# Kernel optimization log

Hardware: AMD Instinct MI355X
Metric: run time of the kernel (lower is better)

## Reference

```python
import jax, jax.numpy as jnp
import numpy as np
import math

B, S, D, H = 2, 2048, 2048, 16
HD = D // H  # head_dim = 128
NEG = -9e15


def setup_inputs() -> dict:
    key = jax.random.key(0)
    k1, k2, k3 = jax.random.split(key, 3)
    x = jax.random.normal(k1, (B, S, D), dtype=jnp.float32)
    Wqkv = jax.random.normal(k2, (D, 3 * D), dtype=jnp.float32) * (1.0 / math.sqrt(D))
    bqkv = jnp.zeros((3 * D,), dtype=jnp.float32)
    Wo = jax.random.normal(k3, (D, D), dtype=jnp.float32) * (1.0 / math.sqrt(D))
    bo = jnp.zeros((D,), dtype=jnp.float32)
    return {"x": x, "Wqkv": Wqkv, "bqkv": bqkv, "Wo": Wo, "bo": bo}


def reference(x, Wqkv, bqkv, Wo, bo):
    b, s, d = x.shape
    # fused QKV projection
    qkv = x @ Wqkv + bqkv                       # [B,S,3D]
    qkv = qkv.reshape(b, s, H, 3 * HD)          # per-head interleaved q|k|v
    qkv = qkv.transpose(0, 2, 1, 3)             # [B,H,S,3*HD]
    q, k, v = jnp.split(qkv, 3, axis=-1)        # each [B,H,S,HD]
    scale = 1.0 / math.sqrt(HD)
    logits = jnp.einsum('bhqd,bhkd->bhqk', q, k) * scale  # [B,H,S,S]
    causal = jnp.tril(jnp.ones((s, s), dtype=bool))[None, None]
    logits = jnp.where(causal, logits, NEG)
    score = jax.nn.softmax(logits, axis=-1)
    attn = jnp.einsum('bhqk,bhkd->bhqd', score, v)         # [B,H,S,HD]
    attn = attn.transpose(0, 2, 1, 3).reshape(b, s, d)
    return attn @ Wo + bo
```

## Files before the change

kernel.cpp:

```cpp
#include <hip/hip_runtime.h>
#include <stdint.h>

#define DEV static __device__ __forceinline__

typedef _Float16 half8 __attribute__((ext_vector_type(8)));
typedef _Float16 half4 __attribute__((ext_vector_type(4)));
typedef float f32x4 __attribute__((ext_vector_type(4)));

constexpr int Bc = 2, Sc = 2048, Dc = 2048, Hc = 16, HDc = 128;
constexpr int D3c = 3 * Dc;
constexpr int Mc = Bc * Sc;

DEV void gl_lds16(const void* g, void* l) {
    __builtin_amdgcn_global_load_lds(
        (const __attribute__((address_space(1))) unsigned int*)g,
        (__attribute__((address_space(3))) unsigned int*)l,
        16, 0, 0);
}

DEV void transpose_tile(const float* __restrict__ in, _Float16* __restrict__ out,
                        int R, int C, int bx, int by, float (*ls)[65], int t)
{
    const int r0 = by * 64, c0 = bx * 64;
    const int rr = t >> 6, cc = t & 63;
#pragma unroll
    for (int i = 0; i < 16; ++i) {
        int r = i * 4 + rr;
        ls[r][cc] = in[(size_t)(r0 + r) * C + c0 + cc];
    }
    __syncthreads();
#pragma unroll
    for (int i = 0; i < 16; ++i) {
        int r = i * 4 + rr;
        out[(size_t)(c0 + r) * R + r0 + cc] = (_Float16)ls[cc][r];
    }
}

__global__ __launch_bounds__(256) void preproc_kernel(
    const float* __restrict__ x, const float* __restrict__ Wqkv,
    const float* __restrict__ Wo,
    _Float16* __restrict__ xb, _Float16* __restrict__ wt1, _Float16* __restrict__ wt2)
{
    __shared__ float ls[64][65];
    const int bid = blockIdx.x, t = threadIdx.x;
    if (bid < 4096) {
        int i = bid * 256 + t;
        const float4* p = (const float4*)x;
        float4 a = p[i * 2], b = p[i * 2 + 1];
        half8 hv;
        hv[0] = (_Float16)a.x; hv[1] = (_Float16)a.y; hv[2] = (_Float16)a.z; hv[3] = (_Float16)a.w;
        hv[4] = (_Float16)b.x; hv[5] = (_Float16)b.y; hv[6] = (_Float16)b.z; hv[7] = (_Float16)b.w;
        *(half8*)(xb + (size_t)i * 8) = hv;
    } else if (bid < 4096 + 3072) {
        int tb = bid - 4096;
        transpose_tile(Wqkv, wt1, Dc, D3c, tb % 96, tb / 96, ls, t);
    } else {
        int tb = bid - 7168;
        transpose_tile(Wo, wt2, Dc, Dc, tb & 31, tb >> 5, ls, t);
    }
}

__global__ __launch_bounds__(256) void transpose_v_kernel(
    const uint16_t* __restrict__ qkv, uint16_t* __restrict__ vt)
{
    __shared__ uint32_t ls[64][65];
    const int t = threadIdx.x;
    const int s0 = blockIdx.x * 64, d0 = blockIdx.y * 64, bh = blockIdx.z;
    const int b = bh >> 4, h = bh & 15;
    const int rr = t >> 6, cc = t & 63;
#pragma unroll
    for (int i = 0; i < 16; ++i) {
        int r = i * 4 + rr;
        ls[r][cc] = qkv[(size_t)(b * Sc + s0 + r) * D3c + h * 384 + 256 + d0 + cc];
    }
    __syncthreads();
#pragma unroll
    for (int i = 0; i < 16; ++i) {
        int r = i * 4 + rr;
        vt[(size_t)(bh * HDc + d0 + r) * Sc + s0 + cc] = (uint16_t)ls[cc][r];
    }
}

template <int BF16OUT>
__global__ __launch_bounds__(256, 2) void gemm_bt_kernel(
    const _Float16* __restrict__ A, const _Float16* __restrict__ Bt,
    const float* __restrict__ bias, void* __restrict__ Cout,
    int M, int N, int K)
{
    __shared__ __align__(16) char smem[32768];
    char* sA = smem;
    char* sB = smem + 16384;
    const int t = threadIdx.x, w = t >> 6, lane = t & 63;
    const int quad = lane >> 4, l15 = lane & 15;
    const int wr = w >> 1, wc = w & 1;
    const int n0 = blockIdx.x * 128, m0 = blockIdx.y * 128;

    const f32x4 vzero = {0.f, 0.f, 0.f, 0.f};
    f32x4 acc[4][4];
#pragma unroll
    for (int i = 0; i < 4; ++i)
#pragma unroll
        for (int j = 0; j < 4; ++j) acc[i][j] = vzero;

    const int kiters = K >> 6;
    for (int kk = 0; kk < kiters; ++kk) {
#pragma unroll
        for (int i = 0; i < 4; ++i) {
            int c = i * 256 + t;
            int row = c >> 3, kbs = c & 7, kact = kbs ^ (row & 7);
            gl_lds16(A + (size_t)(m0 + row) * K + kk * 64 + kact * 8,
                     sA + (i * 256 + w * 64) * 16);
        }
#pragma unroll
        for (int i = 0; i < 4; ++i) {
            int c = i * 256 + t;
            int row = c >> 3, kbs = c & 7, kact = kbs ^ (row & 7);
            gl_lds16(Bt + (size_t)(n0 + row) * K + kk * 64 + kact * 8,
                     sB + (i * 256 + w * 64) * 16);
        }
        __syncthreads();
#pragma unroll
        for (int ks = 0; ks < 2; ++ks) {
            half8 af[4], bf[4];
#pragma unroll
            for (int mt = 0; mt < 4; ++mt) {
                int row = wr * 64 + mt * 16 + l15;
                int kact = (ks * 4 + quad) ^ (l15 & 7);
                af[mt] = *(const half8*)(sA + row * 128 + kact * 16);
            }
#pragma unroll
            for (int nt = 0; nt < 4; ++nt) {
                int row = wc * 64 + nt * 16 + l15;
                int kact = (ks * 4 + quad) ^ (l15 & 7);
                bf[nt] = *(const half8*)(sB + row * 128 + kact * 16);
            }
#pragma unroll
            for (int mt = 0; mt < 4; ++mt)
#pragma unroll
                for (int nt = 0; nt < 4; ++nt)
                    acc[mt][nt] = __builtin_amdgcn_mfma_f32_16x16x32_f16(
                        af[mt], bf[nt], acc[mt][nt], 0, 0, 0);
        }
        __syncthreads();
    }

#pragma unroll
    for (int nt = 0; nt < 4; ++nt) {
        int col = n0 + wc * 64 + nt * 16 + l15;
        float bv = bias[col];
#pragma unroll
        for (int mt = 0; mt < 4; ++mt)
#pragma unroll
            for (int r = 0; r < 4; ++r) {
                int row = m0 + wr * 64 + mt * 16 + quad * 4 + r;
                float v = acc[mt][nt][r] + bv;
                if (BF16OUT) ((_Float16*)Cout)[(size_t)row * N + col] = (_Float16)v;
                else         ((float*)Cout)[(size_t)row * N + col] = v;
            }
    }
}

__global__ __launch_bounds__(256, 3) void flash_kernel(
    const _Float16* __restrict__ qkv, const _Float16* __restrict__ vt,
    _Float16* __restrict__ attn)
{
    __shared__ __align__(16) char smem[34816];
    char* sK = smem;
    char* sV = smem + 16384;

    const int t = threadIdx.x, w = t >> 6, lane = t & 63;
    const int quad = lane >> 4, l15 = lane & 15;
    const int bh = blockIdx.x;
    const int qt = 15 - blockIdx.y;
    const int b = bh >> 4, h = bh & 15;
    const int q0 = qt * 128;
    const int qw = q0 + w * 32;

    half8 qf[2][4];
#pragma unroll
    for (int g = 0; g < 2; ++g)
#pragma unroll
        for (int ks = 0; ks < 4; ++ks) {
            const _Float16* p = qkv + (size_t)(b * Sc + qw + g * 16 + l15) * D3c +
                                h * 384 + ks * 32 + quad * 8;
            qf[g][ks] = *(const half8*)p;
        }

    const f32x4 vzero = {0.f, 0.f, 0.f, 0.f};
    f32x4 o[2][8];
#pragma unroll
    for (int g = 0; g < 2; ++g)
#pragma unroll
        for (int dt = 0; dt < 8; ++dt) o[g][dt] = vzero;
    float m_st[2] = {-1e30f, -1e30f}, l_st[2] = {0.f, 0.f};

    const float kScale = 0.08838834764831845f * 1.4426950408889634f;
    const int nkt = 2 * qt + 2;
    const int nkt_w = (qw + 95) >> 6;

    for (int kt = 0; kt < nkt; ++kt) {
#pragma unroll
        for (int i = 0; i < 4; ++i) {
            int c = i * 256 + t;
            int row = c >> 4, kbs = c & 15, kact = kbs ^ (row & 15);
            gl_lds16(qkv + (size_t)(b * Sc + kt * 64 + row) * D3c + h * 384 + 128 + kact * 8,
                     sK + (i * 256 + w * 64) * 16);
        }
#pragma unroll
        for (int i = 0; i < 4; ++i) {
            int c = i * 256 + t;
            int row = c >> 3, kbs = c & 7, kact = kbs ^ (row & 7);
            gl_lds16(vt + (size_t)(bh * HDc + row) * Sc + kt * 64 + kact * 8,
                     sV + (i * 256 + w * 64) * 16);
        }
        __syncthreads();

        if (kt < nkt_w) {
            f32x4 sf[2][4];
#pragma unroll
            for (int g = 0; g < 2; ++g)
#pragma unroll
                for (int kb = 0; kb < 4; ++kb) sf[g][kb] = vzero;
#pragma unroll
            for (int ks = 0; ks < 4; ++ks) {
#pragma unroll
                for (int kb = 0; kb < 4; ++kb) {
                    int row = kb * 16 + l15;
                    int slot = (ks * 4 + quad) ^ l15;
                    half8 kf = *(const half8*)(sK + row * 256 + slot * 16);
                    sf[0][kb] = __builtin_amdgcn_mfma_f32_16x16x32_f16(kf, qf[0][ks], sf[0][kb], 0, 0, 0);
                    sf[1][kb] = __builtin_amdgcn_mfma_f32_16x16x32_f16(kf, qf[1][ks], sf[1][kb], 0, 0, 0);
                }
            }

            half4 pb[2][4];
#pragma unroll
            for (int g = 0; g < 2; ++g) {
                const int qcol = qw + g * 16 + l15;
                const bool domask = (kt * 64 + 63 > qw + g * 16);
                float rm = -1e30f;
#pragma unroll
                for (int kb = 0; kb < 4; ++kb)
#pragma unroll
                    for (int r = 0; r < 4; ++r) {
                        float v = sf[g][kb][r] * kScale;
                        if (domask) {
                            int col = kt * 64 + kb * 16 + quad * 4 + r;
                            if (col > qcol) v = -1e30f;
                        }
                        sf[g][kb][r] = v;
                        rm = fmaxf(rm, v);
                    }
                rm = fmaxf(rm, __shfl_xor(rm, 16, 64));
                rm = fmaxf(rm, __shfl_xor(rm, 32, 64));
                float mn = fmaxf(m_st[g], rm);
                float alpha = __builtin_amdgcn_exp2f(m_st[g] - mn);
                m_st[g] = mn;

                float rs = 0.f;
#pragma unroll
                for (int kb = 0; kb < 4; ++kb)
#pragma unroll
                    for (int r = 0; r < 4; ++r) {
                        float p = __builtin_amdgcn_exp2f(sf[g][kb][r] - mn);
                        rs += p;
                        pb[g][kb][r] = (_Float16)p;
                    }
                rs += __shfl_xor(rs, 16, 64);
                rs += __shfl_xor(rs, 32, 64);
                l_st[g] = l_st[g] * alpha + rs;
#pragma unroll
                for (int dt = 0; dt < 8; ++dt)
#pragma unroll
                    for (int r = 0; r < 4; ++r) o[g][dt][r] *= alpha;
            }

#pragma unroll
            for (int kb = 0; kb < 4; ++kb) {
#pragma unroll
                for (int dt = 0; dt < 8; ++dt) {
                    int row = dt * 16 + l15;
                    int slot = (kb * 2 + (quad >> 1)) ^ (l15 & 7);
                    half4 vf = *(const half4*)(sV + row * 128 + slot * 16 + (quad & 1) * 8);
                    o[0][dt] = __builtin_amdgcn_mfma_f32_16x16x16f16(vf, pb[0][kb], o[0][dt], 0, 0, 0);
                    o[1][dt] = __builtin_amdgcn_mfma_f32_16x16x16f16(vf, pb[1][kb], o[1][dt], 0, 0, 0);
                }
            }
        }
        __syncthreads();
    }

    char* sO = smem;
#pragma unroll
    for (int g = 0; g < 2; ++g) {
        float linv = 1.0f / l_st[g];
#pragma unroll
        for (int dt = 0; dt < 8; ++dt) {
            half4 hv;
#pragma unroll
            for (int r = 0; r < 4; ++r) hv[r] = (_Float16)(o[g][dt][r] * linv);
            *(half4*)(sO + (w * 32 + g * 16 + l15) * 272 + (dt * 16 + quad * 4) * 2) = hv;
        }
    }
    __syncthreads();
#pragma unroll
    for (int i = 0; i < 8; ++i) {
        int q = i * 16 + (t >> 4);
        int d = (t & 15) * 8;
        half8 hv = *(const half8*)(sO + q * 272 + d * 2);
        *(half8*)(attn + (size_t)(b * Sc + q0 + q) * Dc + h * HDc + d) = hv;
    }
}

extern "C" void kernel_launch(void* const* d_in, const int* in_sizes, int n_in,
                              void* d_out, int out_size, void* d_ws, size_t ws_size,
                              hipStream_t stream)
{
    (void)in_sizes; (void)n_in; (void)out_size; (void)ws_size;
    const float* x    = (const float*)d_in[0];
    const float* Wqkv = (const float*)d_in[1];
    const float* bqkv = (const float*)d_in[2];
    const float* Wo   = (const float*)d_in[3];
    const float* bo   = (const float*)d_in[4];
    float* out = (float*)d_out;

    _Float16* xb  = (_Float16*)d_ws;
    _Float16* wt1 = xb  + (size_t)Mc * Dc;
    _Float16* wt2 = wt1 + (size_t)D3c * Dc;
    _Float16* qkv = wt2 + (size_t)Dc * Dc;
    _Float16* vtg  = wt1;
    _Float16* attn = xb;

    preproc_kernel<<<8192, 256, 0, stream>>>(x, Wqkv, Wo, xb, wt1, wt2);
    gemm_bt_kernel<1><<<dim3(D3c / 128, Mc / 128), 256, 0, stream>>>(
        xb, wt1, bqkv, qkv, Mc, D3c, Dc);
    transpose_v_kernel<<<dim3(Sc / 64, 2, Bc * Hc), 256, 0, stream>>>(
        (const uint16_t*)qkv, (uint16_t*)vtg);
    flash_kernel<<<dim3(Bc * Hc, 16), 256, 0, stream>>>(qkv, vtg, attn);
    gemm_bt_kernel<0><<<dim3(Dc / 128, Mc / 128), 256, 0, stream>>>(
        attn, wt2, bo, out, Mc, Dc, Dc);
}
```

Measured before the change: 409.2 us.

## Restructure flash attention into single-wave blocks with balanced causal work ordering

Result: slower. 418.9 us (+2.3%).

```diff
diff --git a/kernel.cpp b/kernel.cpp
--- a/kernel.cpp
+++ b/kernel.cpp
@@ -17,6 +17,8 @@
         (__attribute__((address_space(3))) unsigned int*)l,
         16, 0, 0);
 }
+#define FENCE_VM   asm volatile("s_waitcnt vmcnt(0)" ::: "memory")
+#define FENCE_LGKM asm volatile("s_waitcnt lgkmcnt(0)" ::: "memory")
 
 DEV void transpose_tile(const float* __restrict__ in, _Float16* __restrict__ out,
                         int R, int C, int bx, int by, float (*ls)[65], int t)
@@ -160,30 +162,34 @@
     }
 }
 
-__global__ __launch_bounds__(256, 3) void flash_kernel(
+__global__ __launch_bounds__(64, 2) void flash_kernel(
     const _Float16* __restrict__ qkv, const _Float16* __restrict__ vt,
     _Float16* __restrict__ attn)
 {
-    __shared__ __align__(16) char smem[34816];
+    __shared__ __align__(16) char smem[16384];
     char* sK = smem;
-    char* sV = smem + 16384;
-
-    const int t = threadIdx.x, w = t >> 6, lane = t & 63;
+    char* sV = smem + 8192;
+
+    const int lane = threadIdx.x & 63;
     const int quad = lane >> 4, l15 = lane & 15;
-    const int bh = blockIdx.x;
-    const int qt = 15 - blockIdx.y;
+
+    const int task = blockIdx.x;
+    const int p = task >> 1;
+    const int idx = (task & 1) ? (2047 - p) : p;
+    const int bh = idx & 31;
+    const int qi = idx >> 5;
+    const int qw = (63 - qi) * 32;
     const int b = bh >> 4, h = bh & 15;
-    const int q0 = qt * 128;
-    const int qw = q0 + w * 32;
+    const int iters = (qw >> 5) + 1;
 
     half8 qf[2][4];
 #pragma unroll
     for (int g = 0; g < 2; ++g)
 #pragma unroll
         for (int ks = 0; ks < 4; ++ks) {
-            const _Float16* p = qkv + (size_t)(b * Sc + qw + g * 16 + l15) * D3c +
-                                h * 384 + ks * 32 + quad * 8;
-            qf[g][ks] = *(const half8*)p;
+            const _Float16* ptr = qkv + (size_t)(b * Sc + qw + g * 16 + l15) * D3c +
+                                  h * 384 + ks * 32 + quad * 8;
+            qf[g][ks] = *(const half8*)ptr;
         }
 
     const f32x4 vzero = {0.f, 0.f, 0.f, 0.f};
@@ -195,120 +201,121 @@
     float m_st[2] = {-1e30f, -1e30f}, l_st[2] = {0.f, 0.f};
 
     const float kScale = 0.08838834764831845f * 1.4426950408889634f;
-    const int nkt = 2 * qt + 2;
-    const int nkt_w = (qw + 95) >> 6;
-
-    for (int kt = 0; kt < nkt; ++kt) {
-#pragma unroll
-        for (int i = 0; i < 4; ++i) {
-            int c = i * 256 + t;
+
+    for (int kt = 0; kt < iters; ++kt) {
+        const int kv0 = kt * 32;
+        FENCE_LGKM;
+#pragma unroll
+        for (int i = 0; i < 8; ++i) {
+            int c = i * 64 + lane;
             int row = c >> 4, kbs = c & 15, kact = kbs ^ (row & 15);
-            gl_lds16(qkv + (size_t)(b * Sc + kt * 64 + row) * D3c + h * 384 + 128 + kact * 8,
-                     sK + (i * 256 + w * 64) * 16);
-        }
-#pragma unroll
-        for (int i = 0; i < 4; ++i) {
-            int c = i * 256 + t;
-            int row = c >> 3, kbs = c & 7, kact = kbs ^ (row & 7);
-            gl_lds16(vt + (size_t)(bh * HDc + row) * Sc + kt * 64 + kact * 8,
-                     sV + (i * 256 + w * 64) * 16);
-        }
-        __syncthreads();
-
-        if (kt < nkt_w) {
-            f32x4 sf[2][4];
-#pragma unroll
-            for (int g = 0; g < 2; ++g)
-#pragma unroll
-                for (int kb = 0; kb < 4; ++kb) sf[g][kb] = vzero;
-#pragma unroll
-            for (int ks = 0; ks < 4; ++ks) {
-#pragma unroll
-                for (int kb = 0; kb < 4; ++kb) {
-                    int row = kb * 16 + l15;
-                    int slot = (ks * 4 + quad) ^ l15;
-                    half8 kf = *(const half8*)(sK + row * 256 + slot * 16);
-                    sf[0][kb] = __builtin_amdgcn_mfma_f32_16x16x32_f16(kf, qf[0][ks], sf[0][kb], 0, 0, 0);
-                    sf[1][kb] = __builtin_amdgcn_mfma_f32_16x16x32_f16(kf, qf[1][ks], sf[1][kb], 0, 0, 0);
+            gl_lds16(qkv + (size_t)(b * Sc + kv0 + row) * D3c + h * 384 + 128 + kact * 8,
+                     sK + i * 1024);
+        }
+#pragma unroll
+        for (int i = 0; i < 8; ++i) {
+            int c = i * 64 + lane;
+            int row = c >> 2, kbs = c & 3;
+            int kact = kbs ^ (row & 3) ^ ((row >> 2) & 3);
+            gl_lds16(vt + (size_t)(bh * HDc + row) * Sc + kv0 + kact * 8,
+                     sV + i * 1024);
+        }
+        FENCE_VM;
+
+        f32x4 sf[2][2];
+#pragma unroll
+        for (int g = 0; g < 2; ++g)
+#pragma unroll
+            for (int kb = 0; kb < 2; ++kb) sf[g][kb] = vzero;
+#pragma unroll
+        for (int ks = 0; ks < 4; ++ks) {
+#pragma unroll
+            for (int kb = 0; kb < 2; ++kb) {
+                int row = kb * 16 + l15;
+                int phys = (ks * 4 + quad) ^ l15;
+                half8 kf = *(const half8*)(sK + row * 256 + phys * 16);
+                sf[0][kb] = __builtin_amdgcn_mfma_f32_16x16x32_f16(kf, qf[0][ks], sf[0][kb], 0, 0, 0);
+                sf[1][kb] = __builtin_amdgcn_mfma_f32_16x16x32_f16(kf, qf[1][ks], sf[1][kb], 0, 0, 0);
+            }
+        }
+
+        const bool last = (kt == iters - 1);
+        half4 pb[2][2];
+#pragma unroll
+        for (int g = 0; g < 2; ++g) {
+            const int qcol = qw + g * 16 + l15;
+            float rm = -1e30f;
+#pragma unroll
+            for (int kb = 0; kb < 2; ++kb)
+#pragma unroll
+                for (int r = 0; r < 4; ++r) {
+                    float v = sf[g][kb][r] * kScale;
+                    if (last) {
+                        int col = kv0 + kb * 16 + quad * 4 + r;
+                        if (col > qcol) v = -1e30f;
+                    }
+                    sf[g][kb][r] = v;
+                    rm = fmaxf(rm, v);
                 }
-            }
-
-            half4 pb[2][4];
-#pragma unroll
-            for (int g = 0; g < 2; ++g) {
-                const int qcol = qw + g * 16 + l15;
-                const bool domask = (kt * 64 + 63 > qw + g * 16);
-                float rm = -1e30f;
-#pragma unroll
-                for (int kb = 0; kb < 4; ++kb)
-#pragma unroll
-                    for (int r = 0; r < 4; ++r) {
-                        float v = sf[g][kb][r] * kScale;
-                        if (domask) {
-                            int col = kt * 64 + kb * 16 + quad * 4 + r;
-                            if (col > qcol) v = -1e30f;
-                        }
-                        sf[g][kb][r] = v;
-                        rm = fmaxf(rm, v);
-                    }
-                rm = fmaxf(rm, __shfl_xor(rm, 16, 64));
-                rm = fmaxf(rm, __shfl_xor(rm, 32, 64));
-                float mn = fmaxf(m_st[g], rm);
-                float alpha = __builtin_amdgcn_exp2f(m_st[g] - mn);
-                m_st[g] = mn;
-
-                float rs = 0.f;
-#pragma unroll
-                for (int kb = 0; kb < 4; ++kb)
-#pragma unroll
-                    for (int r = 0; r < 4; ++r) {
-                        float p = __builtin_amdgcn_exp2f(sf[g][kb][r] - mn);
-                        rs += p;
-                        pb[g][kb][r] = (_Float16)p;
-                    }
-                rs += __shfl_xor(rs, 16, 64);
-                rs += __shfl_xor(rs, 32, 64);
-                l_st[g] = l_st[g] * alpha + rs;
-#pragma unroll
-                for (int dt = 0; dt < 8; ++dt)
-#pragma unroll
-                    for (int r = 0; r < 4; ++r) o[g][dt][r] *= alpha;
-            }
-
-#pragma unroll
-            for (int kb = 0; kb < 4; ++kb) {
-#pragma unroll
-                for (int dt = 0; dt < 8; ++dt) {
-                    int row = dt * 16 + l15;
-                    int slot = (kb * 2 + (quad >> 1)) ^ (l15 & 7);
-                    half4 vf = *(const half4*)(sV + row * 128 + slot * 16 + (quad & 1) * 8);
-                    o[0][dt] = __builtin_amdgcn_mfma_f32_16x16x16f16(vf, pb[0][kb], o[0][dt], 0, 0, 0);
-                    o[1][dt] = __builtin_amdgcn_mfma_f32_16x16x16f16(vf, pb[1][kb], o[1][dt], 0, 0, 0);
+            rm = fmaxf(rm, __shfl_xor(rm, 16));
+            rm = fmaxf(rm, __shfl_xor(rm, 32));
+            float mn = fmaxf(m_st[g], rm);
+            float alpha = __builtin_amdgcn_exp2f(m_st[g] - mn);
+            m_st[g] = mn;
+
+            float rs = 0.f;
+#pragma unroll
+            for (int kb = 0; kb < 2; ++kb)
+#pragma unroll
+                for (int r = 0; r < 4; ++r) {
+                    float pe = __builtin_amdgcn_exp2f(sf[g][kb][r] - mn);
+                    rs += pe;
+                    pb[g][kb][r] = (_Float16)pe;
                 }
-            }
-        }
-        __syncthreads();
-    }
-
-    char* sO = smem;
+            rs += __shfl_xor(rs, 16);
+            rs += __shfl_xor(rs, 32);
+            l_st[g] = l_st[g] * alpha + rs;
+#pragma unroll
+            for (int dt = 0; dt < 8; ++dt)
+#pragma unroll
+                for (int r = 0; r < 4; ++r) o[g][dt][r] *= alpha;
+        }
+
+#pragma unroll
+        for (int kb = 0; kb < 2; ++kb) {
+#pragma unroll
+            for (int dt = 0; dt < 8; ++dt) {
+                int row = dt * 16 + l15;
+                int phys = (kb * 2 + (quad >> 1)) ^ (l15 & 3) ^ ((l15 >> 2) & 3);
+                half4 vf = *(const half4*)(sV + row * 64 + phys * 16 + (quad & 1) * 8);
+                o[0][dt] = __builtin_amdgcn_mfma_f32_16x16x16f16(vf, pb[0][kb], o[0][dt], 0, 0, 0);
+                o[1][dt] = __builtin_amdgcn_mfma_f32_16x16x16f16(vf, pb[1][kb], o[1][dt], 0, 0, 0);
+            }
+        }
+    }
+
+    FENCE_LGKM;
 #pragma unroll
     for (int g = 0; g < 2; ++g) {
         float linv = 1.0f / l_st[g];
+        int qh = g * 16 + l15;
 #pragma unroll
         for (int dt = 0; dt < 8; ++dt) {
             half4 hv;
 #pragma unroll
             for (int r = 0; r < 4; ++r) hv[r] = (_Float16)(o[g][dt][r] * linv);
-            *(half4*)(sO + (w * 32 + g * 16 + l15) * 272 + (dt * 16 + quad * 4) * 2) = hv;
-        }
-    }
-    __syncthreads();
+            int logical = dt * 2 + (quad >> 1);
+            int phys = logical ^ l15;
+            *(half4*)(smem + qh * 256 + phys * 16 + (quad & 1) * 8) = hv;
+        }
+    }
+    FENCE_LGKM;
 #pragma unroll
     for (int i = 0; i < 8; ++i) {
-        int q = i * 16 + (t >> 4);
-        int d = (t & 15) * 8;
-        half8 hv = *(const half8*)(sO + q * 272 + d * 2);
-        *(half8*)(attn + (size_t)(b * Sc + q0 + q) * Dc + h * HDc + d) = hv;
+        int row = i * 4 + quad;
+        int phys = l15 ^ (row & 15);
+        half8 hv = *(const half8*)(smem + row * 256 + phys * 16);
+        *(half8*)(attn + (size_t)(b * Sc + qw + row) * Dc + h * HDc + l15 * 8) = hv;
     }
 }
 
@@ -336,7 +343,7 @@
         xb, wt1, bqkv, qkv, Mc, D3c, Dc);
     transpose_v_kernel<<<dim3(Sc / 64, 2, Bc * Hc), 256, 0, stream>>>(
         (const uint16_t*)qkv, (uint16_t*)vtg);
-    flash_kernel<<<dim3(Bc * Hc, 16), 256, 0, stream>>>(qkv, vtg, attn);
+    flash_kernel<<<2048, 64, 0, stream>>>(qkv, vtg, attn);
     gemm_bt_kernel<0><<<dim3(Dc / 128, Mc / 128), 256, 0, stream>>>(
         attn, wt2, bo, out, Mc, Dc, Dc);
 }
```
